# Performance work log

Hardware: AMD Instinct MI355X
Metric: run time of the kernel (lower is better)

Reference implementation:

```python
import jax, jax.numpy as jnp
import numpy as np

NUM_HEADS = 16
HEAD_DIM = 128
QUERY_DIM = 2048
SCALE = HEAD_DIM ** -0.5


def setup_inputs() -> dict:
    key = jax.random.key(0)
    ks = jax.random.split(key, 11)
    B, L, D = 2, 2048, QUERY_DIM
    HD = NUM_HEADS * HEAD_DIM
    s = 0.02
    return {
        "x_q": jax.random.normal(ks[0], (B, L, D), jnp.float32),
        "x_k": jax.random.normal(ks[1], (B, L, D), jnp.float32),
        "x_v": jax.random.normal(ks[2], (B, L, D), jnp.float32),
        "Wq": jax.random.normal(ks[3], (D, HD), jnp.float32) * s,
        "bq": jnp.zeros((HD,), jnp.float32),
        "Wk": jax.random.normal(ks[4], (D, HD), jnp.float32) * s,
        "bk": jnp.zeros((HD,), jnp.float32),
        "Wv": jax.random.normal(ks[5], (D, HD), jnp.float32) * s,
        "bv": jnp.zeros((HD,), jnp.float32),
        "Wo": jax.random.normal(ks[6], (HD, D), jnp.float32) * s,
        "bo": jnp.zeros((D,), jnp.float32),
    }


def _split_heads(x):  # [b, l, h*d] -> [b, h, l, d]
    b, l, _ = x.shape
    return x.reshape(b, l, NUM_HEADS, HEAD_DIM).transpose(0, 2, 1, 3)


def reference(x_q, x_k, x_v, Wq, bq, Wk, bk, Wv, bv, Wo, bo):
    # Note: the torch module constructs norm_q/norm_k but NEVER applies them in forward.
    q = _split_heads(x_q @ Wq + bq)  # [b, h, l, d]
    k = _split_heads(x_k @ Wk + bk)
    v = _split_heads(x_v @ Wv + bv)
    scores = jnp.einsum("bhid,bhjd->bhij", q, k) * SCALE
    probs = jax.nn.softmax(scores, axis=-1)
    o = jnp.einsum("bhij,bhjd->bhid", probs, v)  # [b, h, l, d]
    b, h, l, d = o.shape
    o = o.transpose(0, 2, 1, 3).reshape(b, l, h * d)
    return o @ Wo + bo
```

## Files before the change

kernel.cpp:

```cpp
#include <hip/hip_runtime.h>


typedef _Float16 f16;
typedef __attribute__((ext_vector_type(8))) _Float16 f16x8;
typedef __attribute__((ext_vector_type(4))) _Float16 f16x4;
typedef __attribute__((ext_vector_type(4))) float f32x4;
typedef __attribute__((ext_vector_type(4))) unsigned int u32x4;

#define QSCALE (0.08838834764831845f * 1.4426950408889634f)
#define SWZ3(r) (((r) & 3) | (((r) >> 1) & 4))
#define SWZV(r) ((r) & 7)

static __device__ __forceinline__ void gload16(void* lds, const void* g) {
  __builtin_amdgcn_global_load_lds(
      (__attribute__((address_space(1))) void*)g,
      (__attribute__((address_space(3))) void*)lds, 16, 0, 0);
}

__global__ __launch_bounds__(256) void cvt_x_kernel(
    const float* __restrict__ x0, const float* __restrict__ x1,
    const float* __restrict__ x2, f16* __restrict__ out) {
  const float* x = blockIdx.z == 0 ? x0 : (blockIdx.z == 1 ? x1 : x2);
  f16* o = out + (size_t)blockIdx.z * 8388608;
  size_t i = ((size_t)blockIdx.x * 256 + threadIdx.x) * 8;
  f32x4 a = *(const f32x4*)(x + i);
  f32x4 b = *(const f32x4*)(x + i + 4);
  f16x8 r;
  r[0] = (f16)a[0]; r[1] = (f16)a[1]; r[2] = (f16)a[2]; r[3] = (f16)a[3];
  r[4] = (f16)b[0]; r[5] = (f16)b[1]; r[6] = (f16)b[2]; r[7] = (f16)b[3];
  *(f16x8*)(o + i) = r;
}

__global__ __launch_bounds__(256) void cvt_w_kernel(
    const float* __restrict__ w0, const float* __restrict__ w1,
    const float* __restrict__ w2, const float* __restrict__ w3,
    f16* __restrict__ out) {
  const float* W = blockIdx.z == 0 ? w0 : blockIdx.z == 1 ? w1
                 : blockIdx.z == 2 ? w2 : w3;
  f16* WT = out + (size_t)blockIdx.z * 4194304;
  __shared__ f16 tile[64][68];
  const int tx = threadIdx.x & 15, ty = threadIdx.x >> 4;
  const int k0 = blockIdx.y * 64, n0 = blockIdx.x * 64;
#pragma unroll
  for (int i = 0; i < 4; ++i) {
    int r = ty + i * 16;
    f32x4 v = *(const f32x4*)(W + (size_t)(k0 + r) * 2048 + n0 + tx * 4);
    tile[r][tx * 4 + 0] = (f16)v[0]; tile[r][tx * 4 + 1] = (f16)v[1];
    tile[r][tx * 4 + 2] = (f16)v[2]; tile[r][tx * 4 + 3] = (f16)v[3];
  }
  __syncthreads();
#pragma unroll
  for (int i = 0; i < 4; ++i) {
    int n = ty + i * 16;
    f16x4 o;
    o[0] = tile[tx * 4 + 0][n]; o[1] = tile[tx * 4 + 1][n];
    o[2] = tile[tx * 4 + 2][n]; o[3] = tile[tx * 4 + 3][n];
    *(f16x4*)(WT + (size_t)(n0 + n) * 2048 + k0 + tx * 4) = o;
  }
}

__global__ __launch_bounds__(256) void gemm_qkv_kernel(
    const f16* __restrict__ Abase, const f16* __restrict__ Btbase,
    f16* __restrict__ Obase, const float* __restrict__ b0,
    const float* __restrict__ b1, const float* __restrict__ b2) {
  const int z = blockIdx.z;
  const f16* A  = Abase  + (size_t)z * 8388608;
  const f16* Bt = Btbase + (size_t)z * 4194304;
  f16* Oz = Obase + (size_t)z * 8388608;
  const float* bias = z == 0 ? b0 : z == 1 ? b1 : b2;
  const float qsc = z == 0 ? QSCALE : 1.0f;
  const int tid = threadIdx.x, lane = tid & 63, w = tid >> 6;
  const int wm = w >> 1, wn = w & 1;
  const int bm = blockIdx.y, bn = blockIdx.x;
  const int l15 = lane & 15, lg = lane >> 4;
  __shared__ alignas(16) f16 As[128 * 32];
  __shared__ alignas(16) f16 Bs[128 * 32];
  f32x4 acc[4][4];
#pragma unroll
  for (int i = 0; i < 4; ++i)
#pragma unroll
    for (int j = 0; j < 4; ++j) acc[i][j] = (f32x4)0.f;

  for (int kt = 0; kt < 64; ++kt) {
    __syncthreads();
#pragma unroll
    for (int i = 0; i < 2; ++i) {
      int c = i * 4 + w;
      int phys = c * 1024 + lane * 16;
      int row = phys >> 6, colb = phys & 63;
      gload16((char*)As + c * 1024,
              (const char*)A + ((size_t)(bm * 128 + row) * 2048 + kt * 32) * 2 + colb);
      gload16((char*)Bs + c * 1024,
              (const char*)Bt + ((size_t)(bn * 128 + row) * 2048 + kt * 32) * 2 + colb);
    }
    __syncthreads();
    f16x8 af[4], bf[4];
#pragma unroll
    for (int i = 0; i < 4; ++i)
      af[i] = *(const f16x8*)(As + (wm * 64 + i * 16 + l15) * 32 + lg * 8);
#pragma unroll
    for (int j = 0; j < 4; ++j)
      bf[j] = *(const f16x8*)(Bs + (wn * 64 + j * 16 + l15) * 32 + lg * 8);
#pragma unroll
    for (int i = 0; i < 4; ++i)
#pragma unroll
      for (int j = 0; j < 4; ++j)
        acc[i][j] = __builtin_amdgcn_mfma_f32_16x16x32_f16(af[i], bf[j], acc[i][j], 0, 0, 0);
  }
#pragma unroll
  for (int i = 0; i < 4; ++i)
#pragma unroll
    for (int j = 0; j < 4; ++j) {
      int col = bn * 128 + wn * 64 + j * 16 + l15;
      int h = col >> 7, d = col & 127;
      float bv = bias[col];
#pragma unroll
      for (int r = 0; r < 4; ++r) {
        int rowg = bm * 128 + wm * 64 + i * 16 + lg * 4 + r;
        int b_ = rowg >> 11, lpos = rowg & 2047;
        Oz[(size_t)(b_ * 16 + h) * 262144 + (size_t)lpos * 128 + d] =
            (f16)((acc[i][j][r] + bv) * qsc);
      }
    }
}

__global__ __launch_bounds__(256) void gemm_out_kernel(
    const f16* __restrict__ A, const f16* __restrict__ Bt,
    float* __restrict__ Out, const float* __restrict__ bias) {
  const int tid = threadIdx.x, lane = tid & 63, w = tid >> 6;
  const int wm = w >> 1, wn = w & 1;
  const int bm = blockIdx.y, bn = blockIdx.x;
  const int l15 = lane & 15, lg = lane >> 4;
  __shared__ alignas(16) f16 As[128 * 32];
  __shared__ alignas(16) f16 Bs[128 * 32];
  f32x4 acc[4][4];
#pragma unroll
  for (int i = 0; i < 4; ++i)
#pragma unroll
    for (int j = 0; j < 4; ++j) acc[i][j] = (f32x4)0.f;

  for (int kt = 0; kt < 64; ++kt) {
    __syncthreads();
#pragma unroll
    for (int i = 0; i < 2; ++i) {
      int c = i * 4 + w;
      int phys = c * 1024 + lane * 16;
      int row = phys >> 6, colb = phys & 63;
      gload16((char*)As + c * 1024,
              (const char*)A + ((size_t)(bm * 128 + row) * 2048 + kt * 32) * 2 + colb);
      gload16((char*)Bs + c * 1024,
              (const char*)Bt + ((size_t)(bn * 128 + row) * 2048 + kt * 32) * 2 + colb);
    }
    __syncthreads();
    f16x8 af[4], bf[4];
#pragma unroll
    for (int i = 0; i < 4; ++i)
      af[i] = *(const f16x8*)(As + (wm * 64 + i * 16 + l15) * 32 + lg * 8);
#pragma unroll
    for (int j = 0; j < 4; ++j)
      bf[j] = *(const f16x8*)(Bs + (wn * 64 + j * 16 + l15) * 32 + lg * 8);
#pragma unroll
    for (int i = 0; i < 4; ++i)
#pragma unroll
      for (int j = 0; j < 4; ++j)
        acc[i][j] = __builtin_amdgcn_mfma_f32_16x16x32_f16(af[i], bf[j], acc[i][j], 0, 0, 0);
  }
#pragma unroll
  for (int i = 0; i < 4; ++i)
#pragma unroll
    for (int j = 0; j < 4; ++j) {
      int col = bn * 128 + wn * 64 + j * 16 + l15;
      float bv = bias[col];
#pragma unroll
      for (int r = 0; r < 4; ++r) {
        int rowg = bm * 128 + wm * 64 + i * 16 + lg * 4 + r;
        Out[(size_t)rowg * 2048 + col] = acc[i][j][r] + bv;
      }
    }
}

__global__ __launch_bounds__(256) void tr_v_kernel(const f16* __restrict__ v,
                                                   f16* __restrict__ vtout) {
  const int bh = blockIdx.z;
  const f16* V = v + (size_t)bh * 262144;
  f16* VT = vtout + (size_t)bh * 262144;
  __shared__ f16 tile[64][68];
  const int tx = threadIdx.x & 15, ty = threadIdx.x >> 4;
  const int l0 = blockIdx.x * 64, d0 = blockIdx.y * 64;
#pragma unroll
  for (int i = 0; i < 4; ++i) {
    int r = ty + i * 16;
    f16x4 val = *(const f16x4*)(V + (size_t)(l0 + r) * 128 + d0 + tx * 4);
    tile[r][tx * 4 + 0] = val[0]; tile[r][tx * 4 + 1] = val[1];
    tile[r][tx * 4 + 2] = val[2]; tile[r][tx * 4 + 3] = val[3];
  }
  __syncthreads();
#pragma unroll
  for (int i = 0; i < 4; ++i) {
    int d = ty + i * 16;
    f16x4 o;
    o[0] = tile[tx * 4 + 0][d]; o[1] = tile[tx * 4 + 1][d];
    o[2] = tile[tx * 4 + 2][d]; o[3] = tile[tx * 4 + 3][d];
    *(f16x4*)(VT + (size_t)(d0 + d) * 2048 + l0 + tx * 4) = o;
  }
}

__global__ __launch_bounds__(512, 4) void attn_kernel(
    const f16* __restrict__ q, const f16* __restrict__ k,
    const f16* __restrict__ vt, f16* __restrict__ o) {
  const int orig = blockIdx.y * 16 + blockIdx.x;
  const int swz = (orig & 7) * 64 + (orig >> 3);
  const int qt = swz & 15, bh = swz >> 4;
  const int tid = threadIdx.x, lane = tid & 63, w = tid >> 6;
  const int l15 = lane & 15, lg = lane >> 4;
  const f16* Qb = q + (size_t)bh * 262144 + (size_t)qt * 128 * 128;
  const char* Kb = (const char*)(k + (size_t)bh * 262144);
  const char* Vtb = (const char*)(vt + (size_t)bh * 262144);
  __shared__ alignas(16) char sm[65536];

  f16x8 qf[4];
#pragma unroll
  for (int ks = 0; ks < 4; ++ks)
    qf[ks] = *(const f16x8*)(Qb + (w * 16 + l15) * 128 + ks * 32 + lg * 8);

  f32x4 oacc[8];
#pragma unroll
  for (int df = 0; df < 8; ++df) oacc[df] = (f32x4)0.f;
  float mrow = -1e30f, ps = 0.f;
  const int rA = ((l15 >> 2) << 3) + (l15 & 3);

#define STAGE(T, B)                                                          \
  {                                                                          \
    char* Ks_ = sm + (B) * 32768;                                            \
    char* Vs_ = Ks_ + 16384;                                                 \
    _Pragma("unroll") for (int i = 0; i < 2; ++i) {                          \
      int c = i * 8 + w;                                                     \
      int phys = c * 1024 + lane * 16;                                       \
      {                                                                      \
        int row = phys >> 8, pcol = phys & 255;                              \
        int lcol = pcol ^ (SWZ3(row) << 4);                                  \
        gload16(Ks_ + c * 1024, Kb + (size_t)((T) * 64 + row) * 256 + lcol); \
      }                                                                      \
      {                                                                      \
        int row = phys >> 7, pcol = phys & 127;                              \
        int lcol = pcol ^ (SWZV(row) << 4);                                  \
        gload16(Vs_ + c * 1024, Vtb + (size_t)row * 4096 + (T) * 128 + lcol);\
      }                                                                      \
    }                                                                        \
  }

  STAGE(0, 0);
  int cur = 0;
  for (int t = 0; t < 32; ++t) {
    __syncthreads();
    if (t < 31) STAGE(t + 1, cur ^ 1);
    const char* Ks = sm + cur * 32768;
    const char* Vs = Ks + 16384;

    f32x4 s[4];
#pragma unroll
    for (int nf = 0; nf < 4; ++nf) s[nf] = (f32x4)0.f;
    __builtin_amdgcn_s_setprio(1);
#pragma unroll
    for (int ks = 0; ks < 4; ++ks) {
      f16x8 kf[4];
#pragma unroll
      for (int nf = 0; nf < 4; ++nf) {
        int row = ((nf & 1) << 5) + ((nf >> 1) << 2) + rA;
        int colb = (ks * 64 + lg * 16) ^ (SWZ3(row) << 4);
        kf[nf] = *(const f16x8*)(Ks + row * 256 + colb);
      }
#pragma unroll
      for (int nf = 0; nf < 4; ++nf)
        s[nf] = __builtin_amdgcn_mfma_f32_16x16x32_f16(kf[nf], qf[ks], s[nf], 0, 0, 0);
    }
    __builtin_amdgcn_s_setprio(0);

    unsigned int pk[2][4];
    {
      float m0 = fmaxf(fmaxf(s[0][0], s[0][1]), fmaxf(s[0][2], s[0][3]));
      float m1 = fmaxf(fmaxf(s[1][0], s[1][1]), fmaxf(s[1][2], s[1][3]));
      float m2 = fmaxf(fmaxf(s[2][0], s[2][1]), fmaxf(s[2][2], s[2][3]));
      float m3 = fmaxf(fmaxf(s[3][0], s[3][1]), fmaxf(s[3][2], s[3][3]));
      float mx = fmaxf(fmaxf(m0, m1), fmaxf(m2, m3));
      mx = fmaxf(mx, __shfl_xor(mx, 16));
      mx = fmaxf(mx, __shfl_xor(mx, 32));
      if (!__all(mx <= mrow + 8.f)) {
        float mnew = fmaxf(mrow, mx);
        float sc = exp2f(mrow - mnew);
        mrow = mnew;
        ps *= sc;
#pragma unroll
        for (int r = 0; r < 4; ++r) {
          float scr = __shfl(sc, (lane & 48) | (lg * 4 + r));
#pragma unroll
          for (int df = 0; df < 8; ++df) oacc[df][r] *= scr;
        }
      }
      float m = mrow;
      float psum = 0.f;
#pragma unroll
      for (int nf = 0; nf < 4; ++nf)
#pragma unroll
        for (int h = 0; h < 2; ++h) {
          float p0 = exp2f(s[nf][2 * h] - m);
          float p1 = exp2f(s[nf][2 * h + 1] - m);
          psum += p0 + p1;
          pk[nf & 1][(nf >> 1) * 2 + h] =
              __builtin_bit_cast(unsigned int, __builtin_amdgcn_cvt_pkrtz(p0, p1));
        }
      ps += psum;
    }

    __builtin_amdgcn_s_setprio(1);
#pragma unroll
    for (int kvs = 0; kvs < 2; ++kvs) {
      f16x8 pa = __builtin_bit_cast(f16x8, *(const u32x4*)pk[kvs]);
#pragma unroll
      for (int df = 0; df < 8; ++df) {
        int row = df * 16 + l15;
        int colb = (kvs * 64 + lg * 16) ^ (SWZV(row) << 4);
        f16x8 vb = *(const f16x8*)(Vs + row * 128 + colb);
        oacc[df] = __builtin_amdgcn_mfma_f32_16x16x32_f16(pa, vb, oacc[df], 0, 0, 0);
      }
    }
    __builtin_amdgcn_s_setprio(0);
    cur ^= 1;
  }

  const int b_ = bh >> 4, h_ = bh & 15;
  f16* Ob = o + (size_t)b_ * 4194304 + (size_t)qt * 128 * 2048 + h_ * 128;
  float lr = ps;
  lr += __shfl_xor(lr, 16);
  lr += __shfl_xor(lr, 32);
  float inv = 1.f / lr;
#pragma unroll
  for (int r = 0; r < 4; ++r) {
    float invr = __shfl(inv, (lane & 48) | (lg * 4 + r));
    int rl = w * 16 + lg * 4 + r;
#pragma unroll
    for (int df = 0; df < 8; ++df)
      Ob[(size_t)rl * 2048 + df * 16 + l15] = (f16)(oacc[df][r] * invr);
  }
#undef STAGE
}

extern "C" void kernel_launch(void* const* d_in, const int* in_sizes, int n_in,
                              void* d_out, int out_size, void* d_ws, size_t ws_size,
                              hipStream_t stream) {
  const float* xq = (const float*)d_in[0];
  const float* xk = (const float*)d_in[1];
  const float* xv = (const float*)d_in[2];
  const float* Wq = (const float*)d_in[3];
  const float* bq = (const float*)d_in[4];
  const float* Wk = (const float*)d_in[5];
  const float* bk = (const float*)d_in[6];
  const float* Wv = (const float*)d_in[7];
  const float* bv = (const float*)d_in[8];
  const float* Wo = (const float*)d_in[9];
  const float* bo = (const float*)d_in[10];

  char* ws = (char*)d_ws;
  f16* xh   = (f16*)(ws);
  f16* wt   = (f16*)(ws + 50331648);
  f16* qkv  = (f16*)(ws + 83886080);
  f16* vtb  = (f16*)(ws);
  f16* oatt = (f16*)(ws + 16777216);
  float* outp = (float*)d_out;

  hipLaunchKernelGGL(cvt_x_kernel, dim3(4096, 1, 3), dim3(256), 0, stream,
                     xq, xk, xv, xh);
  hipLaunchKernelGGL(cvt_w_kernel, dim3(32, 32, 4), dim3(256), 0, stream,
                     Wq, Wk, Wv, Wo, wt);
  hipLaunchKernelGGL(gemm_qkv_kernel, dim3(16, 32, 3), dim3(256), 0, stream,
                     xh, wt, qkv, bq, bk, bv);
  hipLaunchKernelGGL(tr_v_kernel, dim3(32, 2, 32), dim3(256), 0, stream,
                     qkv + (size_t)2 * 8388608, vtb);
  hipLaunchKernelGGL(attn_kernel, dim3(16, 32), dim3(512), 0, stream,
                     qkv, qkv + (size_t)8388608, vtb, oatt);
  hipLaunchKernelGGL(gemm_out_kernel, dim3(16, 32), dim3(256), 0, stream,
                     oatt, wt + (size_t)3 * 4194304, outp, bo);
}
```

Measured before the change: 328.6 us.

## Retile QKV GEMM to 256x256 with double-buffered swizzled LDS pipeline

Rewrites the QKV projection GEMM to use 512-thread blocks computing 256x256 tiles with a K-step of 64. The next K-tile is loaded into a second LDS buffer while the current one is consumed, and an XOR swizzle on the LDS layout avoids bank conflicts. MFMA issue is raised in priority with s_setprio. The intent is more data reuse per block, fewer barriers per FLOP and overlap of global loads with compute. The cost is 128KB of LDS per block and higher register pressure from 32 accumulators per wave, which limits occupancy. The grid shrinks to 384 blocks, which may leave some CUs unevenly loaded.

```diff
diff --git a/kernel.cpp b/kernel.cpp
--- a/kernel.cpp
+++ b/kernel.cpp
@@ -59,7 +59,7 @@
   }
 }
 
-__global__ __launch_bounds__(256) void gemm_qkv_kernel(
+__global__ __launch_bounds__(512, 2) void gemm_qkv_kernel(
     const f16* __restrict__ Abase, const f16* __restrict__ Btbase,
     f16* __restrict__ Obase, const float* __restrict__ b0,
     const float* __restrict__ b1, const float* __restrict__ b2) {
@@ -70,58 +70,98 @@
   const float* bias = z == 0 ? b0 : z == 1 ? b1 : b2;
   const float qsc = z == 0 ? QSCALE : 1.0f;
   const int tid = threadIdx.x, lane = tid & 63, w = tid >> 6;
-  const int wm = w >> 1, wn = w & 1;
+  const int wm = w >> 2, wn = w & 3;
   const int bm = blockIdx.y, bn = blockIdx.x;
   const int l15 = lane & 15, lg = lane >> 4;
-  __shared__ alignas(16) f16 As[128 * 32];
-  __shared__ alignas(16) f16 Bs[128 * 32];
-  f32x4 acc[4][4];
-#pragma unroll
-  for (int i = 0; i < 4; ++i)
+  __shared__ alignas(16) char smb[131072];
+
+  f32x4 acc[8][4];
+#pragma unroll
+  for (int i = 0; i < 8; ++i)
 #pragma unroll
     for (int j = 0; j < 4; ++j) acc[i][j] = (f32x4)0.f;
 
-  for (int kt = 0; kt < 64; ++kt) {
-    __syncthreads();
-#pragma unroll
-    for (int i = 0; i < 2; ++i) {
-      int c = i * 4 + w;
-      int phys = c * 1024 + lane * 16;
-      int row = phys >> 6, colb = phys & 63;
-      gload16((char*)As + c * 1024,
-              (const char*)A + ((size_t)(bm * 128 + row) * 2048 + kt * 32) * 2 + colb);
-      gload16((char*)Bs + c * 1024,
-              (const char*)Bt + ((size_t)(bn * 128 + row) * 2048 + kt * 32) * 2 + colb);
-    }
-    __syncthreads();
-    f16x8 af[4], bf[4];
-#pragma unroll
-    for (int i = 0; i < 4; ++i)
-      af[i] = *(const f16x8*)(As + (wm * 64 + i * 16 + l15) * 32 + lg * 8);
-#pragma unroll
-    for (int j = 0; j < 4; ++j)
-      bf[j] = *(const f16x8*)(Bs + (wn * 64 + j * 16 + l15) * 32 + lg * 8);
-#pragma unroll
-    for (int i = 0; i < 4; ++i)
-#pragma unroll
-      for (int j = 0; j < 4; ++j)
-        acc[i][j] = __builtin_amdgcn_mfma_f32_16x16x32_f16(af[i], bf[j], acc[i][j], 0, 0, 0);
-  }
-#pragma unroll
-  for (int i = 0; i < 4; ++i)
+#define GSTAGE(KT, C_)                                                        \
+  {                                                                           \
+    char* Ab_ = smb + (C_) * 65536;                                           \
+    char* Bb_ = Ab_ + 32768;                                                  \
+    _Pragma("unroll") for (int p = 0; p < 4; ++p) {                           \
+      int L = p * 8192 + tid * 16;                                            \
+      int row = L >> 7, pcol = L & 127;                                       \
+      int scol = pcol ^ ((row & 7) << 4);                                     \
+      gload16(Ab_ + L,                                                        \
+              (const char*)A + ((size_t)(bm * 256 + row) * 2048 + (KT) * 64) * 2 + scol); \
+      gload16(Bb_ + L,                                                        \
+              (const char*)Bt + ((size_t)(bn * 256 + row) * 2048 + (KT) * 64) * 2 + scol); \
+    }                                                                         \
+  }
+
+  GSTAGE(0, 0);
+#pragma unroll 1
+  for (int kt = 0; kt < 32; ++kt) {
+    const int c = kt & 1;
+    if (kt < 31) {
+      GSTAGE(kt + 1, c ^ 1);
+      asm volatile("s_waitcnt vmcnt(8)" ::: "memory");
+    } else {
+      asm volatile("s_waitcnt vmcnt(0)" ::: "memory");
+    }
+    __builtin_amdgcn_s_barrier();
+
+    const char* Ab = smb + c * 65536;
+    const char* Bb = Ab + 32768;
+    f16x8 bf[4][2];
+#pragma unroll
+    for (int p = 0; p < 4; ++p) {
+      f16x8 af[2][2];
+#pragma unroll
+      for (int pp = 0; pp < 2; ++pp)
+#pragma unroll
+        for (int h = 0; h < 2; ++h) {
+          int row = wm * 128 + (p * 2 + pp) * 16 + l15;
+          af[pp][h] = *(const f16x8*)(Ab + row * 128 +
+                                      ((h * 64 + lg * 16) ^ ((row & 7) << 4)));
+        }
+      if (p == 0) {
+#pragma unroll
+        for (int j = 0; j < 4; ++j)
+#pragma unroll
+          for (int h = 0; h < 2; ++h) {
+            int row = wn * 64 + j * 16 + l15;
+            bf[j][h] = *(const f16x8*)(Bb + row * 128 +
+                                       ((h * 64 + lg * 16) ^ ((row & 7) << 4)));
+          }
+      }
+      __builtin_amdgcn_s_setprio(1);
+#pragma unroll
+      for (int pp = 0; pp < 2; ++pp)
+#pragma unroll
+        for (int j = 0; j < 4; ++j)
+#pragma unroll
+          for (int h = 0; h < 2; ++h)
+            acc[p * 2 + pp][j] = __builtin_amdgcn_mfma_f32_16x16x32_f16(
+                af[pp][h], bf[j][h], acc[p * 2 + pp][j], 0, 0, 0);
+      __builtin_amdgcn_s_setprio(0);
+      __builtin_amdgcn_s_barrier();
+    }
+  }
+
+#pragma unroll
+  for (int i = 0; i < 8; ++i)
 #pragma unroll
     for (int j = 0; j < 4; ++j) {
-      int col = bn * 128 + wn * 64 + j * 16 + l15;
+      int col = bn * 256 + wn * 64 + j * 16 + l15;
       int h = col >> 7, d = col & 127;
       float bv = bias[col];
 #pragma unroll
       for (int r = 0; r < 4; ++r) {
-        int rowg = bm * 128 + wm * 64 + i * 16 + lg * 4 + r;
+        int rowg = bm * 256 + wm * 128 + i * 16 + lg * 4 + r;
         int b_ = rowg >> 11, lpos = rowg & 2047;
         Oz[(size_t)(b_ * 16 + h) * 262144 + (size_t)lpos * 128 + d] =
             (f16)((acc[i][j][r] + bv) * qsc);
       }
     }
+#undef GSTAGE
 }
 
 __global__ __launch_bounds__(256) void gemm_out_kernel(
@@ -372,7 +412,7 @@
                      xq, xk, xv, xh);
   hipLaunchKernelGGL(cvt_w_kernel, dim3(32, 32, 4), dim3(256), 0, stream,
                      Wq, Wk, Wv, Wo, wt);
-  hipLaunchKernelGGL(gemm_qkv_kernel, dim3(16, 32, 3), dim3(256), 0, stream,
+  hipLaunchKernelGGL(gemm_qkv_kernel, dim3(8, 16, 3), dim3(512), 0, stream,
                      xh, wt, qkv, bq, bk, bv);
   hipLaunchKernelGGL(tr_v_kernel, dim3(32, 2, 32), dim3(256), 0, stream,
                      qkv + (size_t)2 * 8388608, vtb);
```

After: 321.1 us. 1.02x faster.
